# Kernel tuning notes

Hardware: AMD Instinct MI355X
Metric: run time of the kernel (lower is better)

The kernel has to match this reference:

```python
import jax, jax.numpy as jnp
import numpy as np

# FCHL19 hyperparameters (from init_kwargs defaults)
NSPEC = 4
RCUT = 6.0
NRS2 = 24
NRS3 = 20
ETA2 = 0.32
ETA3 = 2.7
TWO_BODY_DECAY = 1.8
THREE_BODY_WEIGHT = float(np.sqrt(2.7 / np.pi) * 13.4)  # sqrt(eta3/pi)*13.4, as in __init__
THREE_BODY_DECAY = 0.57
PI = float(np.pi)
NPAIRS = NSPEC * (NSPEC + 1) // 2  # 10 unordered element pairs
RS2 = jnp.linspace(0.0, RCUT, NRS2 + 1)[1:]
RS3 = jnp.linspace(0.0, RCUT, NRS3 + 1)[1:]


def setup_inputs() -> dict:
    key = jax.random.key(0)
    k1, k2, k3 = jax.random.split(key, 3)
    B, A = 64, 48
    X = jax.random.uniform(k1, (B, A, 3), jnp.float32, 0.0, 12.0)  # coords in 12 A box
    Z = jax.random.randint(k2, (B, A), 0, NSPEC, dtype=jnp.int32)  # species indices into [1,6,7,8]
    atom_counts = jax.random.randint(k3, (B,), 24, A + 1, dtype=jnp.int32)
    atomIDs = (jnp.arange(B * A, dtype=jnp.int32) % A)
    molIDs = (jnp.arange(B * A, dtype=jnp.int32) // A)
    return {"X": X, "Z": Z, "atomIDs": atomIDs, "molIDs": molIDs, "atom_counts": atom_counts}


def _fchl_rep(X, Z, atom_counts):
    B, A, _ = X.shape
    idx = jnp.arange(A)
    valid = idx[None, :] < atom_counts[:, None]                       # [B,A]
    diff = X[:, :, None, :] - X[:, None, :, :]                        # [B,A,A,3] (X_i - X_j)
    r2 = jnp.sum(diff * diff, axis=-1)
    eye = jnp.eye(A, dtype=bool)
    pmask = valid[:, :, None] & valid[:, None, :] & ~eye              # [B,A,A]
    r = jnp.sqrt(jnp.where(pmask, r2, 1.0))
    within = pmask & (r < RCUT)
    rs = jnp.where(within, r, 1.0)                                    # safe distances
    fc = jnp.where(within, 0.5 * (jnp.cos(PI * rs / RCUT) + 1.0), 0.0)

    # ---- two-body: log-normal radial basis with power-law scaling ----
    s2 = jnp.log1p(ETA2 / (rs * rs))                                  # sigma^2
    mu = jnp.log(rs) - 0.5 * s2
    pref = fc / (rs ** TWO_BODY_DECAY) / (jnp.sqrt(s2) * np.sqrt(2.0 * PI))
    radial2 = (pref[..., None] / RS2) * jnp.exp(
        -(jnp.log(RS2) - mu[..., None]) ** 2 / (2.0 * s2[..., None]))  # [B,A,A,nRs2]
    eoh = jax.nn.one_hot(Z, NSPEC, dtype=X.dtype) * valid[..., None]  # [B,A,S]
    rep2 = jnp.einsum('bijk,bjs->bisk', radial2, eoh).reshape(B, A, NSPEC * NRS2)

    # ---- three-body: ATM-weighted radial x (cos,sin) angular, pairs k>j ----
    rij = rs[:, :, :, None]   # [B,A(i),A(j),1]
    rik = rs[:, :, None, :]   # [B,A(i),1,A(k)]
    rjk = rs[:, None, :, :]   # [B,1,A(j),A(k)]
    cos_i = jnp.einsum('bijx,bikx->bijk', diff, diff) / (rij * rik)
    cos_i = jnp.clip(cos_i, -1.0, 1.0)
    cos_j = (rij * rij + rjk * rjk - rik * rik) / (2.0 * rij * rjk)
    cos_k = (rik * rik + rjk * rjk - rij * rij) / (2.0 * rik * rjk)
    mask3 = (within[:, :, :, None] & within[:, :, None, :]
             & (idx[None, :] > idx[:, None])[None, None, :, :])        # k > j
    ksi3 = THREE_BODY_WEIGHT * (1.0 + 3.0 * cos_i * cos_j * cos_k) \
        / (rij * rik * rjk) ** THREE_BODY_DECAY
    w = jnp.where(mask3, ksi3 * fc[:, :, :, None] * fc[:, :, None, :], 0.0)
    wc = w * cos_i
    ws = w * jnp.sqrt(jnp.clip(1.0 - cos_i * cos_i, 0.0, 1.0))
    d = 0.5 * (rij + rik)                                             # [B,A,A,A]

    # unordered element-pair bin for (Z_j, Z_k)
    ej = Z[:, :, None]
    ek = Z[:, None, :]
    pmin = jnp.minimum(ej, ek)
    pmax = jnp.maximum(ej, ek)
    pidx = pmin * (2 * NSPEC - pmin - 1) // 2 + pmax                  # [B,A,A]
    poh = jax.nn.one_hot(pidx, NPAIRS, dtype=X.dtype)                 # [B,A,A,P]

    def step(carry, Rl):
        rad = jnp.exp(-ETA3 * (d - Rl) ** 2)
        rc = jnp.einsum('bijk,bjkp->bip', wc * rad, poh)
        rsn = jnp.einsum('bijk,bjkp->bip', ws * rad, poh)
        return carry, jnp.stack([rc, rsn], axis=-1)                   # [B,A,P,2]

    _, rep3 = jax.lax.scan(step, 0, RS3)                              # [nRs3,B,A,P,2]
    rep3 = jnp.transpose(rep3, (1, 2, 3, 0, 4)).reshape(B, A, NPAIRS * NRS3 * 2)
    return jnp.concatenate([rep2, rep3], axis=-1)                     # [B,A,496]


def reference(X, Z, atomIDs, molIDs, atom_counts):
    # atomIDs/molIDs are CUDA work-distribution lists; math-irrelevant here.
    return _fchl_rep(X, Z, atom_counts)
```

## Files before the change

### kernel.cpp

```cpp
#include <hip/hip_runtime.h>
#include <math.h>

#define B_MOL 64
#define A_MAX 48
#define NSPEC 4
#define NRS2 24
#define NRS3 20
#define NPAIRS 10
#define REP2 (NSPEC * NRS2)
#define REP3 (NPAIRS * NRS3 * 2)
#define REPTOT (REP2 + REP3)
#define TRIP_CAP 1084

#define RCUT_F 6.0f
#define ETA2_F 0.32f
#define ETA3_F 2.7f
#define PI_F 3.14159265358979323846f
#define W3_F 12.4225780586f
#define SQRT_2PI_F 2.5066282746310002f

__device__ __forceinline__ void decode_tri(int t, int m, int& a_out, int& c_out) {
    const float fm = (float)(2 * m - 1);
    const float disc = fm * fm - 8.0f * (float)t;
    const float sq = __builtin_amdgcn_sqrtf(disc);
    int a = (int)((fm - sq) * 0.5f);
    if (a < 0) a = 0;
    while (a > 0 && (a * (2 * m - 1 - a)) / 2 > t) --a;
    while (((a + 1) * (2 * m - 1 - (a + 1))) / 2 <= t) ++a;
    a_out = a;
    c_out = t - (a * (2 * m - 1 - a)) / 2 + a + 1;
}

__global__ __launch_bounds__(256, 8) void fchl_kernel(
    const float* __restrict__ X, const int* __restrict__ Z,
    const int* __restrict__ atom_counts, float* __restrict__ out)
{
    const int bi = blockIdx.x;
    const int b = bi / A_MAX;
    const int i = bi % A_MAX;
    const int tid = threadIdx.x;

    __shared__ float nb_dx[A_MAX], nb_dy[A_MAX], nb_dz[A_MAX];
    __shared__ float nb_r[A_MAX], nb_r2[A_MAX], nb_rinv[A_MAX];
    __shared__ float nb_fc[A_MAX], nb_mu[A_MAX], nb_i2s2[A_MAX], nb_pref[A_MAX];
    __shared__ int   nb_z[A_MAX];
    __shared__ int   nb_m;
    __shared__ int   bcnt[NPAIRS], bstart[NPAIRS];
    __shared__ unsigned short pq[TRIP_CAP];
    __shared__ float trip_wc[TRIP_CAP], trip_ws[TRIP_CAP], trip_d[TRIP_CAP];

    const int cnt = atom_counts[b];
    float* orow = out + (size_t)bi * REPTOT;

    if (i >= cnt) {
        for (int t = tid; t < REPTOT; t += 256) orow[t] = 0.0f;
        return;
    }

    if (tid < NPAIRS) bcnt[tid] = 0;

    const float xi = X[(b * A_MAX + i) * 3 + 0];
    const float yi = X[(b * A_MAX + i) * 3 + 1];
    const float zi = X[(b * A_MAX + i) * 3 + 2];

    if (tid < 64) {
        const int j = tid;
        bool flag = false;
        float dx = 0.f, dy = 0.f, dz = 0.f, r = 1.f;
        int zj = 0;
        if (j < A_MAX && j < cnt) {
            dx = xi - X[(b * A_MAX + j) * 3 + 0];
            dy = yi - X[(b * A_MAX + j) * 3 + 1];
            dz = zi - X[(b * A_MAX + j) * 3 + 2];
            zj = Z[b * A_MAX + j];
            r = __builtin_amdgcn_sqrtf(dx * dx + dy * dy + dz * dz);
            flag = (j != i) && (r < RCUT_F);
        }
        const unsigned long long mask = __ballot(flag ? 1 : 0);
        if (flag) {
            const int pos = __popcll(mask & ((1ull << tid) - 1ull));
            nb_dx[pos] = dx; nb_dy[pos] = dy; nb_dz[pos] = dz;
            nb_r[pos]  = r;  nb_r2[pos] = r * r;
            nb_rinv[pos] = __builtin_amdgcn_rcpf(r);
            nb_z[pos]  = zj;
            const float fc = 0.5f * (__cosf(PI_F * r * (1.0f / RCUT_F)) + 1.0f);
            const float lr = __logf(r);
            const float s2 = log1pf(ETA2_F / (r * r));
            nb_fc[pos]   = fc;
            nb_mu[pos]   = lr - 0.5f * s2;
            nb_i2s2[pos] = 0.5f * __builtin_amdgcn_rcpf(s2);
            nb_pref[pos] = fc * __expf(-1.8f * lr) *
                           __builtin_amdgcn_rcpf(__builtin_amdgcn_sqrtf(s2) * SQRT_2PI_F);
        }
        if (tid == 0) nb_m = (int)__popcll(mask);
    }
    __syncthreads();
    const int m = nb_m;
    const int ntrip = m * (m - 1) / 2;

    for (int t = tid; t < ntrip; t += 256) {
        int a, c;
        decode_tri(t, m, a, c);
        const int zj = nb_z[a], zk = nb_z[c];
        const int pmn = min(zj, zk), pmx = max(zj, zk);
        const int p = (pmn * (2 * NSPEC - pmn - 1)) / 2 + pmx;
        const int q = atomicAdd(&bcnt[p], 1);
        pq[t] = (unsigned short)(p | (q << 4));
    }
    __syncthreads();
    if (tid < NPAIRS) {
        int s = 0;
        for (int p = 0; p < tid; ++p) s += bcnt[p];
        bstart[tid] = s;
    }
    __syncthreads();

    for (int t = tid; t < ntrip; t += 256) {
        int a, c;
        decode_tri(t, m, a, c);

        const float rij = nb_r[a], rik = nb_r[c];
        const float r2ij = nb_r2[a], r2ik = nb_r2[c];
        const float rinv_a = nb_rinv[a], rinv_c = nb_rinv[c];
        const float djx = nb_dx[a], djy = nb_dy[a], djz = nb_dz[a];
        const float dkx = nb_dx[c], dky = nb_dy[c], dkz = nb_dz[c];

        float cosi = (djx * dkx + djy * dky + djz * dkz) * rinv_a * rinv_c;
        cosi = fminf(1.0f, fmaxf(-1.0f, cosi));

        const float ex = dkx - djx, ey = dky - djy, ez = dkz - djz;
        const float rjk2 = ex * ex + ey * ey + ez * ez;
        const float rjk = __builtin_amdgcn_sqrtf(rjk2);
        const bool w_jk = (rjk < RCUT_F);
        const float rjke  = w_jk ? rjk : 1.0f;
        const float rjke2 = w_jk ? rjk2 : 1.0f;
        const float rinv_jk = w_jk ? __builtin_amdgcn_rcpf(rjk) : 1.0f;

        const float cosj = (r2ij + rjke2 - r2ik) * 0.5f * rinv_a * rinv_jk;
        const float cosk = (r2ik + rjke2 - r2ij) * 0.5f * rinv_c * rinv_jk;

        const float ksi = W3_F * (1.0f + 3.0f * cosi * cosj * cosk)
                        * __expf(-0.57f * __logf(rij * rik * rjke));
        const float w  = ksi * nb_fc[a] * nb_fc[c];
        const float wc = w * cosi;
        const float s1 = fmaxf(1.0f - cosi * cosi, 0.0f);
        const float ws = w * __builtin_amdgcn_sqrtf(s1);
        const float d  = 0.5f * (rij + rik);

        const unsigned short e = pq[t];
        const int slot = bstart[e & 15] + (int)(e >> 4);
        trip_wc[slot] = wc; trip_ws[slot] = ws; trip_d[slot] = d;
    }
    __syncthreads();

    if (tid < NPAIRS * NRS3) {
        const int p = tid / NRS3;
        const int l = tid % NRS3;
        const float Rl = 0.3f * (float)(l + 1);
        const int s0 = bstart[p];
        const int s1 = s0 + bcnt[p];
        float ac = 0.0f, as_ = 0.0f;
        if (s1 > s0) {
            float wcv = trip_wc[s0], wsv = trip_ws[s0], dv = trip_d[s0];
            for (int s = s0 + 1; s < s1; ++s) {
                const float wcn = trip_wc[s];
                const float wsn = trip_ws[s];
                const float dn  = trip_d[s];
                const float dd = dv - Rl;
                const float rad = __expf(-ETA3_F * dd * dd);
                ac  += wcv * rad;
                as_ += wsv * rad;
                wcv = wcn; wsv = wsn; dv = dn;
            }
            const float dd = dv - Rl;
            const float rad = __expf(-ETA3_F * dd * dd);
            ac  += wcv * rad;
            as_ += wsv * rad;
        }
        orow[REP2 + p * (NRS3 * 2) + l * 2 + 0] = ac;
        orow[REP2 + p * (NRS3 * 2) + l * 2 + 1] = as_;
    } else {
        for (int t2 = tid - 200; t2 < REP2; t2 += 56) {
            const int s = t2 / NRS2;
            const int n = t2 % NRS2;
            const float Rn = 0.25f * (float)(n + 1);
            const float logRn = __logf(Rn);
            float acc = 0.0f;
            for (int a = 0; a < m; ++a) {
                if (nb_z[a] == s) {
                    const float dmu = logRn - nb_mu[a];
                    acc += nb_pref[a] * __expf(-dmu * dmu * nb_i2s2[a]);
                }
            }
            orow[t2] = acc * __builtin_amdgcn_rcpf(Rn);
        }
    }
}

extern "C" void kernel_launch(void* const* d_in, const int* in_sizes, int n_in,
                              void* d_out, int out_size, void* d_ws, size_t ws_size,
                              hipStream_t stream) {
    const float* X           = (const float*)d_in[0];
    const int*   Z           = (const int*)d_in[1];
    const int*   atom_counts = (const int*)d_in[4];
    float* out = (float*)d_out;

    fchl_kernel<<<B_MOL * A_MAX, 256, 0, stream>>>(X, Z, atom_counts, out);
}
```

Measured before the change: 74.70 us.

## Map one wavefront per atom and accumulate three-body bins with LDS atomics

Restructures the kernel so each 64-lane wavefront handles one atom, with two atoms per block, replacing the 256-thread block per atom. The two-pass bucket sort of triplets by element pair (counting atomics, prefix sum, scatter) and the separate per-bin reduction are removed. Each lane instead computes a triplet and scatters its 20 radial contributions into a per-wave LDS accumulator with float atomics, starting at a lane-staggered offset to spread bank conflicts. This cuts block-wide barriers and idle threads, but adds many LDS atomic adds and puts all triplet work on 64 lanes per atom.

```diff
diff --git a/kernel.cpp b/kernel.cpp
--- a/kernel.cpp
+++ b/kernel.cpp
@@ -10,7 +10,6 @@
 #define REP2 (NSPEC * NRS2)
 #define REP3 (NPAIRS * NRS3 * 2)
 #define REPTOT (REP2 + REP3)
-#define TRIP_CAP 1084
 
 #define RCUT_F 6.0f
 #define ETA2_F 0.32f
@@ -18,6 +17,8 @@
 #define PI_F 3.14159265358979323846f
 #define W3_F 12.4225780586f
 #define SQRT_2PI_F 2.5066282746310002f
+
+#define WPB 2
 
 __device__ __forceinline__ void decode_tri(int t, int m, int& a_out, int& c_out) {
     const float fm = (float)(2 * m - 1);
@@ -31,169 +32,138 @@
     c_out = t - (a * (2 * m - 1 - a)) / 2 + a + 1;
 }
 
-__global__ __launch_bounds__(256, 8) void fchl_kernel(
+__global__ __launch_bounds__(64 * WPB, 6) void fchl_kernel(
     const float* __restrict__ X, const int* __restrict__ Z,
     const int* __restrict__ atom_counts, float* __restrict__ out)
 {
-    const int bi = blockIdx.x;
+    __shared__ float nb_dx[WPB][A_MAX], nb_dy[WPB][A_MAX], nb_dz[WPB][A_MAX];
+    __shared__ float nb_r[WPB][A_MAX], nb_r2[WPB][A_MAX], nb_rinv[WPB][A_MAX];
+    __shared__ float nb_fc[WPB][A_MAX], nb_mu[WPB][A_MAX];
+    __shared__ float nb_i2s2[WPB][A_MAX], nb_pref[WPB][A_MAX];
+    __shared__ int   nb_z[WPB][A_MAX];
+    __shared__ float acc3[WPB][REP3];
+
+    const int wv   = threadIdx.x >> 6;
+    const int lane = threadIdx.x & 63;
+    const int bi   = blockIdx.x * WPB + wv;
     const int b = bi / A_MAX;
     const int i = bi % A_MAX;
-    const int tid = threadIdx.x;
-
-    __shared__ float nb_dx[A_MAX], nb_dy[A_MAX], nb_dz[A_MAX];
-    __shared__ float nb_r[A_MAX], nb_r2[A_MAX], nb_rinv[A_MAX];
-    __shared__ float nb_fc[A_MAX], nb_mu[A_MAX], nb_i2s2[A_MAX], nb_pref[A_MAX];
-    __shared__ int   nb_z[A_MAX];
-    __shared__ int   nb_m;
-    __shared__ int   bcnt[NPAIRS], bstart[NPAIRS];
-    __shared__ unsigned short pq[TRIP_CAP];
-    __shared__ float trip_wc[TRIP_CAP], trip_ws[TRIP_CAP], trip_d[TRIP_CAP];
-
     const int cnt = atom_counts[b];
     float* orow = out + (size_t)bi * REPTOT;
+    const bool active = (i < cnt);
 
-    if (i >= cnt) {
-        for (int t = tid; t < REPTOT; t += 256) orow[t] = 0.0f;
-        return;
-    }
+    int m = 0;
 
-    if (tid < NPAIRS) bcnt[tid] = 0;
+    if (active) {
+        const float xi = X[(b * A_MAX + i) * 3 + 0];
+        const float yi = X[(b * A_MAX + i) * 3 + 1];
+        const float zi = X[(b * A_MAX + i) * 3 + 2];
 
-    const float xi = X[(b * A_MAX + i) * 3 + 0];
-    const float yi = X[(b * A_MAX + i) * 3 + 1];
-    const float zi = X[(b * A_MAX + i) * 3 + 2];
-
-    if (tid < 64) {
-        const int j = tid;
         bool flag = false;
         float dx = 0.f, dy = 0.f, dz = 0.f, r = 1.f;
         int zj = 0;
-        if (j < A_MAX && j < cnt) {
-            dx = xi - X[(b * A_MAX + j) * 3 + 0];
-            dy = yi - X[(b * A_MAX + j) * 3 + 1];
-            dz = zi - X[(b * A_MAX + j) * 3 + 2];
-            zj = Z[b * A_MAX + j];
+        if (lane < A_MAX && lane < cnt) {
+            dx = xi - X[(b * A_MAX + lane) * 3 + 0];
+            dy = yi - X[(b * A_MAX + lane) * 3 + 1];
+            dz = zi - X[(b * A_MAX + lane) * 3 + 2];
+            zj = Z[b * A_MAX + lane];
             r = __builtin_amdgcn_sqrtf(dx * dx + dy * dy + dz * dz);
-            flag = (j != i) && (r < RCUT_F);
+            flag = (lane != i) && (r < RCUT_F);
         }
         const unsigned long long mask = __ballot(flag ? 1 : 0);
         if (flag) {
-            const int pos = __popcll(mask & ((1ull << tid) - 1ull));
-            nb_dx[pos] = dx; nb_dy[pos] = dy; nb_dz[pos] = dz;
-            nb_r[pos]  = r;  nb_r2[pos] = r * r;
-            nb_rinv[pos] = __builtin_amdgcn_rcpf(r);
-            nb_z[pos]  = zj;
+            const int pos = __popcll(mask & ((1ull << lane) - 1ull));
+            nb_dx[wv][pos] = dx; nb_dy[wv][pos] = dy; nb_dz[wv][pos] = dz;
+            nb_r[wv][pos]  = r;  nb_r2[wv][pos] = r * r;
+            nb_rinv[wv][pos] = __builtin_amdgcn_rcpf(r);
+            nb_z[wv][pos]  = zj;
             const float fc = 0.5f * (__cosf(PI_F * r * (1.0f / RCUT_F)) + 1.0f);
             const float lr = __logf(r);
             const float s2 = log1pf(ETA2_F / (r * r));
-            nb_fc[pos]   = fc;
-            nb_mu[pos]   = lr - 0.5f * s2;
-            nb_i2s2[pos] = 0.5f * __builtin_amdgcn_rcpf(s2);
-            nb_pref[pos] = fc * __expf(-1.8f * lr) *
-                           __builtin_amdgcn_rcpf(__builtin_amdgcn_sqrtf(s2) * SQRT_2PI_F);
+            nb_fc[wv][pos]   = fc;
+            nb_mu[wv][pos]   = lr - 0.5f * s2;
+            nb_i2s2[wv][pos] = 0.5f * __builtin_amdgcn_rcpf(s2);
+            nb_pref[wv][pos] = fc * __expf(-1.8f * lr) *
+                               __builtin_amdgcn_rcpf(__builtin_amdgcn_sqrtf(s2) * SQRT_2PI_F);
         }
-        if (tid == 0) nb_m = (int)__popcll(mask);
-    }
-    __syncthreads();
-    const int m = nb_m;
-    const int ntrip = m * (m - 1) / 2;
-
-    for (int t = tid; t < ntrip; t += 256) {
-        int a, c;
-        decode_tri(t, m, a, c);
-        const int zj = nb_z[a], zk = nb_z[c];
-        const int pmn = min(zj, zk), pmx = max(zj, zk);
-        const int p = (pmn * (2 * NSPEC - pmn - 1)) / 2 + pmx;
-        const int q = atomicAdd(&bcnt[p], 1);
-        pq[t] = (unsigned short)(p | (q << 4));
-    }
-    __syncthreads();
-    if (tid < NPAIRS) {
-        int s = 0;
-        for (int p = 0; p < tid; ++p) s += bcnt[p];
-        bstart[tid] = s;
+        m = (int)__popcll(mask);
+        for (int k2 = lane; k2 < REP3; k2 += 64) acc3[wv][k2] = 0.0f;
     }
     __syncthreads();
 
-    for (int t = tid; t < ntrip; t += 256) {
-        int a, c;
-        decode_tri(t, m, a, c);
-
-        const float rij = nb_r[a], rik = nb_r[c];
-        const float r2ij = nb_r2[a], r2ik = nb_r2[c];
-        const float rinv_a = nb_rinv[a], rinv_c = nb_rinv[c];
-        const float djx = nb_dx[a], djy = nb_dy[a], djz = nb_dz[a];
-        const float dkx = nb_dx[c], dky = nb_dy[c], dkz = nb_dz[c];
-
-        float cosi = (djx * dkx + djy * dky + djz * dkz) * rinv_a * rinv_c;
-        cosi = fminf(1.0f, fmaxf(-1.0f, cosi));
-
-        const float ex = dkx - djx, ey = dky - djy, ez = dkz - djz;
-        const float rjk2 = ex * ex + ey * ey + ez * ez;
-        const float rjk = __builtin_amdgcn_sqrtf(rjk2);
-        const bool w_jk = (rjk < RCUT_F);
-        const float rjke  = w_jk ? rjk : 1.0f;
-        const float rjke2 = w_jk ? rjk2 : 1.0f;
-        const float rinv_jk = w_jk ? __builtin_amdgcn_rcpf(rjk) : 1.0f;
-
-        const float cosj = (r2ij + rjke2 - r2ik) * 0.5f * rinv_a * rinv_jk;
-        const float cosk = (r2ik + rjke2 - r2ij) * 0.5f * rinv_c * rinv_jk;
-
-        const float ksi = W3_F * (1.0f + 3.0f * cosi * cosj * cosk)
-                        * __expf(-0.57f * __logf(rij * rik * rjke));
-        const float w  = ksi * nb_fc[a] * nb_fc[c];
-        const float wc = w * cosi;
-        const float s1 = fmaxf(1.0f - cosi * cosi, 0.0f);
-        const float ws = w * __builtin_amdgcn_sqrtf(s1);
-        const float d  = 0.5f * (rij + rik);
-
-        const unsigned short e = pq[t];
-        const int slot = bstart[e & 15] + (int)(e >> 4);
-        trip_wc[slot] = wc; trip_ws[slot] = ws; trip_d[slot] = d;
-    }
-    __syncthreads();
-
-    if (tid < NPAIRS * NRS3) {
-        const int p = tid / NRS3;
-        const int l = tid % NRS3;
-        const float Rl = 0.3f * (float)(l + 1);
-        const int s0 = bstart[p];
-        const int s1 = s0 + bcnt[p];
-        float ac = 0.0f, as_ = 0.0f;
-        if (s1 > s0) {
-            float wcv = trip_wc[s0], wsv = trip_ws[s0], dv = trip_d[s0];
-            for (int s = s0 + 1; s < s1; ++s) {
-                const float wcn = trip_wc[s];
-                const float wsn = trip_ws[s];
-                const float dn  = trip_d[s];
-                const float dd = dv - Rl;
-                const float rad = __expf(-ETA3_F * dd * dd);
-                ac  += wcv * rad;
-                as_ += wsv * rad;
-                wcv = wcn; wsv = wsn; dv = dn;
-            }
-            const float dd = dv - Rl;
-            const float rad = __expf(-ETA3_F * dd * dd);
-            ac  += wcv * rad;
-            as_ += wsv * rad;
-        }
-        orow[REP2 + p * (NRS3 * 2) + l * 2 + 0] = ac;
-        orow[REP2 + p * (NRS3 * 2) + l * 2 + 1] = as_;
-    } else {
-        for (int t2 = tid - 200; t2 < REP2; t2 += 56) {
+    if (active) {
+        for (int t2 = lane; t2 < REP2; t2 += 64) {
             const int s = t2 / NRS2;
             const int n = t2 % NRS2;
             const float Rn = 0.25f * (float)(n + 1);
             const float logRn = __logf(Rn);
             float acc = 0.0f;
             for (int a = 0; a < m; ++a) {
-                if (nb_z[a] == s) {
-                    const float dmu = logRn - nb_mu[a];
-                    acc += nb_pref[a] * __expf(-dmu * dmu * nb_i2s2[a]);
+                if (nb_z[wv][a] == s) {
+                    const float dmu = logRn - nb_mu[wv][a];
+                    acc += nb_pref[wv][a] * __expf(-dmu * dmu * nb_i2s2[wv][a]);
                 }
             }
             orow[t2] = acc * __builtin_amdgcn_rcpf(Rn);
         }
+
+        const int ntrip = m * (m - 1) / 2;
+        const int l0 = lane % NRS3;
+        for (int t = lane; t < ntrip; t += 64) {
+            int a, c;
+            decode_tri(t, m, a, c);
+
+            const float rij = nb_r[wv][a], rik = nb_r[wv][c];
+            const float r2ij = nb_r2[wv][a], r2ik = nb_r2[wv][c];
+            const float rinv_a = nb_rinv[wv][a], rinv_c = nb_rinv[wv][c];
+            const float djx = nb_dx[wv][a], djy = nb_dy[wv][a], djz = nb_dz[wv][a];
+            const float dkx = nb_dx[wv][c], dky = nb_dy[wv][c], dkz = nb_dz[wv][c];
+
+            float cosi = (djx * dkx + djy * dky + djz * dkz) * rinv_a * rinv_c;
+            cosi = fminf(1.0f, fmaxf(-1.0f, cosi));
+
+            const float ex = dkx - djx, ey = dky - djy, ez = dkz - djz;
+            const float rjk2 = ex * ex + ey * ey + ez * ez;
+            const float rjk = __builtin_amdgcn_sqrtf(rjk2);
+            const bool w_jk = (rjk < RCUT_F);
+            const float rjke  = w_jk ? rjk : 1.0f;
+            const float rjke2 = w_jk ? rjk2 : 1.0f;
+            const float rinv_jk = w_jk ? __builtin_amdgcn_rcpf(rjk) : 1.0f;
+
+            const float cosj = (r2ij + rjke2 - r2ik) * 0.5f * rinv_a * rinv_jk;
+            const float cosk = (r2ik + rjke2 - r2ij) * 0.5f * rinv_c * rinv_jk;
+
+            const float ksi = W3_F * (1.0f + 3.0f * cosi * cosj * cosk)
+                            * __expf(-0.57f * __logf(rij * rik * rjke));
+            const float w  = ksi * nb_fc[wv][a] * nb_fc[wv][c];
+            const float wc = w * cosi;
+            const float s1 = fmaxf(1.0f - cosi * cosi, 0.0f);
+            const float ws = w * __builtin_amdgcn_sqrtf(s1);
+            const float d  = 0.5f * (rij + rik);
+
+            const int zj = nb_z[wv][a], zk = nb_z[wv][c];
+            const int pmn = min(zj, zk), pmx = max(zj, zk);
+            const int p = (pmn * (2 * NSPEC - pmn - 1)) / 2 + pmx;
+            float* accp = &acc3[wv][p * (NRS3 * 2)];
+
+            int l = l0;
+            for (int it = 0; it < NRS3; ++it) {
+                const float Rl = 0.3f * (float)(l + 1);
+                const float dd = d - Rl;
+                const float rad = __expf(-ETA3_F * dd * dd);
+                atomicAdd(&accp[2 * l + 0], wc * rad);
+                atomicAdd(&accp[2 * l + 1], ws * rad);
+                l = (l + 1 == NRS3) ? 0 : l + 1;
+            }
+        }
+    } else {
+        for (int k2 = lane; k2 < REPTOT; k2 += 64) orow[k2] = 0.0f;
+    }
+    __syncthreads();
+
+    if (active) {
+        for (int k2 = lane; k2 < REP3; k2 += 64)
+            orow[REP2 + k2] = acc3[wv][k2];
     }
 }
 
@@ -205,5 +175,5 @@
     const int*   atom_counts = (const int*)d_in[4];
     float* out = (float*)d_out;
 
-    fchl_kernel<<<B_MOL * A_MAX, 256, 0, stream>>>(X, Z, atom_counts, out);
+    fchl_kernel<<<(B_MOL * A_MAX) / WPB, 64 * WPB, 0, stream>>>(X, Z, atom_counts, out);
 }
```

Result: slower. 121.7 us (+62.9%).

## Use single-wavefront blocks and bin triplets via an index list in one pass

Applied to the files above, without the earlier changes.

Shrinks each block from 256 threads to a single 64-lane wavefront, so the neighbour count comes straight from a ballot and no shared broadcast is needed. The triplet loop now computes weights, stores them in natural order and does the pair-bin atomic in the same pass, which removes the second decode pass. A separate scatter then builds a sorted index array that the three-body accumulation reads indirectly. Each block now has a quarter of the threads for the same work, which trades parallelism within a block for fewer redundant decodes. The accumulation loop also pays an extra indirect LDS load for every triplet.

```diff
diff --git a/kernel.cpp b/kernel.cpp
--- a/kernel.cpp
+++ b/kernel.cpp
@@ -31,54 +31,52 @@
     c_out = t - (a * (2 * m - 1 - a)) / 2 + a + 1;
 }
 
-__global__ __launch_bounds__(256, 8) void fchl_kernel(
+__global__ __launch_bounds__(64, 4) void fchl_kernel(
     const float* __restrict__ X, const int* __restrict__ Z,
     const int* __restrict__ atom_counts, float* __restrict__ out)
 {
-    const int bi = blockIdx.x;
-    const int b = bi / A_MAX;
-    const int i = bi % A_MAX;
-    const int tid = threadIdx.x;
-
     __shared__ float nb_dx[A_MAX], nb_dy[A_MAX], nb_dz[A_MAX];
     __shared__ float nb_r[A_MAX], nb_r2[A_MAX], nb_rinv[A_MAX];
     __shared__ float nb_fc[A_MAX], nb_mu[A_MAX], nb_i2s2[A_MAX], nb_pref[A_MAX];
     __shared__ int   nb_z[A_MAX];
-    __shared__ int   nb_m;
-    __shared__ int   bcnt[NPAIRS], bstart[NPAIRS];
+    __shared__ float trip_wc[TRIP_CAP], trip_ws[TRIP_CAP], trip_d[TRIP_CAP];
     __shared__ unsigned short pq[TRIP_CAP];
-    __shared__ float trip_wc[TRIP_CAP], trip_ws[TRIP_CAP], trip_d[TRIP_CAP];
-
+    __shared__ unsigned short sidx[TRIP_CAP];
+    __shared__ int bcnt[NPAIRS], bstart[NPAIRS];
+
+    const int bi = blockIdx.x;
+    const int b = bi / A_MAX;
+    const int i = bi % A_MAX;
+    const int lane = threadIdx.x;
     const int cnt = atom_counts[b];
     float* orow = out + (size_t)bi * REPTOT;
 
     if (i >= cnt) {
-        for (int t = tid; t < REPTOT; t += 256) orow[t] = 0.0f;
+        for (int t = lane; t < REPTOT; t += 64) orow[t] = 0.0f;
         return;
     }
 
-    if (tid < NPAIRS) bcnt[tid] = 0;
+    if (lane < NPAIRS) bcnt[lane] = 0;
 
     const float xi = X[(b * A_MAX + i) * 3 + 0];
     const float yi = X[(b * A_MAX + i) * 3 + 1];
     const float zi = X[(b * A_MAX + i) * 3 + 2];
 
-    if (tid < 64) {
-        const int j = tid;
-        bool flag = false;
+    bool flag = false;
+    {
         float dx = 0.f, dy = 0.f, dz = 0.f, r = 1.f;
         int zj = 0;
-        if (j < A_MAX && j < cnt) {
-            dx = xi - X[(b * A_MAX + j) * 3 + 0];
-            dy = yi - X[(b * A_MAX + j) * 3 + 1];
-            dz = zi - X[(b * A_MAX + j) * 3 + 2];
-            zj = Z[b * A_MAX + j];
+        if (lane < A_MAX && lane < cnt) {
+            dx = xi - X[(b * A_MAX + lane) * 3 + 0];
+            dy = yi - X[(b * A_MAX + lane) * 3 + 1];
+            dz = zi - X[(b * A_MAX + lane) * 3 + 2];
+            zj = Z[b * A_MAX + lane];
             r = __builtin_amdgcn_sqrtf(dx * dx + dy * dy + dz * dz);
-            flag = (j != i) && (r < RCUT_F);
+            flag = (lane != i) && (r < RCUT_F);
         }
         const unsigned long long mask = __ballot(flag ? 1 : 0);
         if (flag) {
-            const int pos = __popcll(mask & ((1ull << tid) - 1ull));
+            const int pos = __popcll(mask & ((1ull << lane) - 1ull));
             nb_dx[pos] = dx; nb_dy[pos] = dy; nb_dz[pos] = dz;
             nb_r[pos]  = r;  nb_r2[pos] = r * r;
             nb_rinv[pos] = __builtin_amdgcn_rcpf(r);
@@ -92,30 +90,27 @@
             nb_pref[pos] = fc * __expf(-1.8f * lr) *
                            __builtin_amdgcn_rcpf(__builtin_amdgcn_sqrtf(s2) * SQRT_2PI_F);
         }
-        if (tid == 0) nb_m = (int)__popcll(mask);
-    }
-    __syncthreads();
-    const int m = nb_m;
+    }
+    const int m = (int)__popcll(__ballot(flag ? 1 : 0));
+    __syncthreads();
+
+    for (int t2 = lane; t2 < REP2; t2 += 64) {
+        const int s = t2 / NRS2;
+        const int n = t2 % NRS2;
+        const float Rn = 0.25f * (float)(n + 1);
+        const float logRn = __logf(Rn);
+        float acc = 0.0f;
+        for (int a = 0; a < m; ++a) {
+            if (nb_z[a] == s) {
+                const float dmu = logRn - nb_mu[a];
+                acc += nb_pref[a] * __expf(-dmu * dmu * nb_i2s2[a]);
+            }
+        }
+        orow[t2] = acc * __builtin_amdgcn_rcpf(Rn);
+    }
+
     const int ntrip = m * (m - 1) / 2;
-
-    for (int t = tid; t < ntrip; t += 256) {
-        int a, c;
-        decode_tri(t, m, a, c);
-        const int zj = nb_z[a], zk = nb_z[c];
-        const int pmn = min(zj, zk), pmx = max(zj, zk);
-        const int p = (pmn * (2 * NSPEC - pmn - 1)) / 2 + pmx;
-        const int q = atomicAdd(&bcnt[p], 1);
-        pq[t] = (unsigned short)(p | (q << 4));
-    }
-    __syncthreads();
-    if (tid < NPAIRS) {
-        int s = 0;
-        for (int p = 0; p < tid; ++p) s += bcnt[p];
-        bstart[tid] = s;
-    }
-    __syncthreads();
-
-    for (int t = tid; t < ntrip; t += 256) {
+    for (int t = lane; t < ntrip; t += 64) {
         int a, c;
         decode_tri(t, m, a, c);
 
@@ -142,58 +137,58 @@
         const float ksi = W3_F * (1.0f + 3.0f * cosi * cosj * cosk)
                         * __expf(-0.57f * __logf(rij * rik * rjke));
         const float w  = ksi * nb_fc[a] * nb_fc[c];
-        const float wc = w * cosi;
         const float s1 = fmaxf(1.0f - cosi * cosi, 0.0f);
-        const float ws = w * __builtin_amdgcn_sqrtf(s1);
-        const float d  = 0.5f * (rij + rik);
-
+
+        trip_wc[t] = w * cosi;
+        trip_ws[t] = w * __builtin_amdgcn_sqrtf(s1);
+        trip_d[t]  = 0.5f * (rij + rik);
+
+        const int zj = nb_z[a], zk = nb_z[c];
+        const int pmn = min(zj, zk), pmx = max(zj, zk);
+        const int p = (pmn * (2 * NSPEC - pmn - 1)) / 2 + pmx;
+        const int q = atomicAdd(&bcnt[p], 1);
+        pq[t] = (unsigned short)(p | (q << 4));
+    }
+    __syncthreads();
+    if (lane < NPAIRS) {
+        int s = 0;
+        for (int p = 0; p < lane; ++p) s += bcnt[p];
+        bstart[lane] = s;
+    }
+    __syncthreads();
+
+    for (int t = lane; t < ntrip; t += 64) {
         const unsigned short e = pq[t];
-        const int slot = bstart[e & 15] + (int)(e >> 4);
-        trip_wc[slot] = wc; trip_ws[slot] = ws; trip_d[slot] = d;
-    }
-    __syncthreads();
-
-    if (tid < NPAIRS * NRS3) {
-        const int p = tid / NRS3;
-        const int l = tid % NRS3;
+        sidx[bstart[e & 15] + (int)(e >> 4)] = (unsigned short)t;
+    }
+    __syncthreads();
+
+    for (int e = lane; e < NPAIRS * NRS3; e += 64) {
+        const int p = e / NRS3;
+        const int l = e % NRS3;
         const float Rl = 0.3f * (float)(l + 1);
         const int s0 = bstart[p];
         const int s1 = s0 + bcnt[p];
         float ac = 0.0f, as_ = 0.0f;
         if (s1 > s0) {
-            float wcv = trip_wc[s0], wsv = trip_ws[s0], dv = trip_d[s0];
+            int idx = sidx[s0];
             for (int s = s0 + 1; s < s1; ++s) {
-                const float wcn = trip_wc[s];
-                const float wsn = trip_ws[s];
-                const float dn  = trip_d[s];
+                const int idxn = sidx[s];
+                const float dv = trip_d[idx];
                 const float dd = dv - Rl;
                 const float rad = __expf(-ETA3_F * dd * dd);
-                ac  += wcv * rad;
-                as_ += wsv * rad;
-                wcv = wcn; wsv = wsn; dv = dn;
+                ac  += trip_wc[idx] * rad;
+                as_ += trip_ws[idx] * rad;
+                idx = idxn;
             }
+            const float dv = trip_d[idx];
             const float dd = dv - Rl;
             const float rad = __expf(-ETA3_F * dd * dd);
-            ac  += wcv * rad;
-            as_ += wsv * rad;
+            ac  += trip_wc[idx] * rad;
+            as_ += trip_ws[idx] * rad;
         }
         orow[REP2 + p * (NRS3 * 2) + l * 2 + 0] = ac;
         orow[REP2 + p * (NRS3 * 2) + l * 2 + 1] = as_;
-    } else {
-        for (int t2 = tid - 200; t2 < REP2; t2 += 56) {
-            const int s = t2 / NRS2;
-            const int n = t2 % NRS2;
-            const float Rn = 0.25f * (float)(n + 1);
-            const float logRn = __logf(Rn);
-            float acc = 0.0f;
-            for (int a = 0; a < m; ++a) {
-                if (nb_z[a] == s) {
-                    const float dmu = logRn - nb_mu[a];
-                    acc += nb_pref[a] * __expf(-dmu * dmu * nb_i2s2[a]);
-                }
-            }
-            orow[t2] = acc * __builtin_amdgcn_rcpf(Rn);
-        }
     }
 }
 
@@ -205,5 +200,5 @@
     const int*   atom_counts = (const int*)d_in[4];
     float* out = (float*)d_out;
 
-    fchl_kernel<<<B_MOL * A_MAX, 256, 0, stream>>>(X, Z, atom_counts, out);
+    fchl_kernel<<<B_MOL * A_MAX, 64, 0, stream>>>(X, Z, atom_counts, out);
 }
```

New measurement: 85.00 us. +13.8%, slower.

## Compute triplet bin slots analytically from per-species ballots, dropping atomic binning pass

Applied to the files above, without the earlier changes.

Replaces the atomic-counting pass that bucketed triplets by element pair with closed-form slot indices. Per-species ballots give each neighbour its rank within its species and the count of each species, so slot offsets and ranks come from arithmetic. This removes one triplet loop, the shared atomics and two block barriers. The radial accumulation loop is also unrolled by two with split accumulators to raise instruction-level parallelism. The bin order inside each pair is now deterministic, which changes the float summation order.

```diff
diff --git a/kernel.cpp b/kernel.cpp
--- a/kernel.cpp
+++ b/kernel.cpp
@@ -35,20 +35,18 @@
     const float* __restrict__ X, const int* __restrict__ Z,
     const int* __restrict__ atom_counts, float* __restrict__ out)
 {
+    __shared__ float nb_dx[A_MAX], nb_dy[A_MAX], nb_dz[A_MAX];
+    __shared__ float nb_r[A_MAX], nb_r2[A_MAX], nb_rinv[A_MAX];
+    __shared__ float nb_fc[A_MAX], nb_mu[A_MAX], nb_i2s2[A_MAX], nb_pref[A_MAX];
+    __shared__ int   nb_z[A_MAX], nb_si[A_MAX];
+    __shared__ float trip_wc[TRIP_CAP], trip_ws[TRIP_CAP], trip_d[TRIP_CAP];
+    __shared__ int   cnt_s[NSPEC];
+    __shared__ int   nb_m;
+
     const int bi = blockIdx.x;
     const int b = bi / A_MAX;
     const int i = bi % A_MAX;
     const int tid = threadIdx.x;
-
-    __shared__ float nb_dx[A_MAX], nb_dy[A_MAX], nb_dz[A_MAX];
-    __shared__ float nb_r[A_MAX], nb_r2[A_MAX], nb_rinv[A_MAX];
-    __shared__ float nb_fc[A_MAX], nb_mu[A_MAX], nb_i2s2[A_MAX], nb_pref[A_MAX];
-    __shared__ int   nb_z[A_MAX];
-    __shared__ int   nb_m;
-    __shared__ int   bcnt[NPAIRS], bstart[NPAIRS];
-    __shared__ unsigned short pq[TRIP_CAP];
-    __shared__ float trip_wc[TRIP_CAP], trip_ws[TRIP_CAP], trip_d[TRIP_CAP];
-
     const int cnt = atom_counts[b];
     float* orow = out + (size_t)bi * REPTOT;
 
@@ -57,32 +55,37 @@
         return;
     }
 
-    if (tid < NPAIRS) bcnt[tid] = 0;
-
-    const float xi = X[(b * A_MAX + i) * 3 + 0];
-    const float yi = X[(b * A_MAX + i) * 3 + 1];
-    const float zi = X[(b * A_MAX + i) * 3 + 2];
-
     if (tid < 64) {
-        const int j = tid;
+        const float xi = X[(b * A_MAX + i) * 3 + 0];
+        const float yi = X[(b * A_MAX + i) * 3 + 1];
+        const float zi = X[(b * A_MAX + i) * 3 + 2];
+
         bool flag = false;
         float dx = 0.f, dy = 0.f, dz = 0.f, r = 1.f;
         int zj = 0;
-        if (j < A_MAX && j < cnt) {
-            dx = xi - X[(b * A_MAX + j) * 3 + 0];
-            dy = yi - X[(b * A_MAX + j) * 3 + 1];
-            dz = zi - X[(b * A_MAX + j) * 3 + 2];
-            zj = Z[b * A_MAX + j];
+        if (tid < A_MAX && tid < cnt) {
+            dx = xi - X[(b * A_MAX + tid) * 3 + 0];
+            dy = yi - X[(b * A_MAX + tid) * 3 + 1];
+            dz = zi - X[(b * A_MAX + tid) * 3 + 2];
+            zj = Z[b * A_MAX + tid];
             r = __builtin_amdgcn_sqrtf(dx * dx + dy * dy + dz * dz);
-            flag = (j != i) && (r < RCUT_F);
-        }
-        const unsigned long long mask = __ballot(flag ? 1 : 0);
+            flag = (tid != i) && (r < RCUT_F);
+        }
+        const unsigned long long ms0 = __ballot(flag && zj == 0);
+        const unsigned long long ms1 = __ballot(flag && zj == 1);
+        const unsigned long long ms2 = __ballot(flag && zj == 2);
+        const unsigned long long ms3 = __ballot(flag && zj == 3);
+        const unsigned long long mask = ms0 | ms1 | ms2 | ms3;
         if (flag) {
-            const int pos = __popcll(mask & ((1ull << tid) - 1ull));
+            const unsigned long long below = (1ull << tid) - 1ull;
+            const int pos = __popcll(mask & below);
             nb_dx[pos] = dx; nb_dy[pos] = dy; nb_dz[pos] = dz;
             nb_r[pos]  = r;  nb_r2[pos] = r * r;
             nb_rinv[pos] = __builtin_amdgcn_rcpf(r);
             nb_z[pos]  = zj;
+            const unsigned long long msp = (zj == 0) ? ms0 : (zj == 1) ? ms1
+                                         : (zj == 2) ? ms2 : ms3;
+            nb_si[pos] = __popcll(msp & below);
             const float fc = 0.5f * (__cosf(PI_F * r * (1.0f / RCUT_F)) + 1.0f);
             const float lr = __logf(r);
             const float s2 = log1pf(ETA2_F / (r * r));
@@ -92,28 +95,25 @@
             nb_pref[pos] = fc * __expf(-1.8f * lr) *
                            __builtin_amdgcn_rcpf(__builtin_amdgcn_sqrtf(s2) * SQRT_2PI_F);
         }
-        if (tid == 0) nb_m = (int)__popcll(mask);
+        if (tid == 0) {
+            cnt_s[0] = (int)__popcll(ms0);
+            cnt_s[1] = (int)__popcll(ms1);
+            cnt_s[2] = (int)__popcll(ms2);
+            cnt_s[3] = (int)__popcll(ms3);
+            nb_m = (int)__popcll(mask);
+        }
     }
     __syncthreads();
-    const int m = nb_m;
+
+    const int m  = nb_m;
+    const int c0 = cnt_s[0], c1 = cnt_s[1], c2 = cnt_s[2], c3 = cnt_s[3];
+    const int S0 = (c0 * (c0 - 1)) >> 1;
+    const int S1 = c0 * c1, S2 = c0 * c2, S3 = c0 * c3;
+    const int S4 = (c1 * (c1 - 1)) >> 1;
+    const int S5 = c1 * c2, S6 = c1 * c3;
+    const int S7 = (c2 * (c2 - 1)) >> 1;
+    const int S8 = c2 * c3;
     const int ntrip = m * (m - 1) / 2;
-
-    for (int t = tid; t < ntrip; t += 256) {
-        int a, c;
-        decode_tri(t, m, a, c);
-        const int zj = nb_z[a], zk = nb_z[c];
-        const int pmn = min(zj, zk), pmx = max(zj, zk);
-        const int p = (pmn * (2 * NSPEC - pmn - 1)) / 2 + pmx;
-        const int q = atomicAdd(&bcnt[p], 1);
-        pq[t] = (unsigned short)(p | (q << 4));
-    }
-    __syncthreads();
-    if (tid < NPAIRS) {
-        int s = 0;
-        for (int p = 0; p < tid; ++p) s += bcnt[p];
-        bstart[tid] = s;
-    }
-    __syncthreads();
 
     for (int t = tid; t < ntrip; t += 256) {
         int a, c;
@@ -142,14 +142,32 @@
         const float ksi = W3_F * (1.0f + 3.0f * cosi * cosj * cosk)
                         * __expf(-0.57f * __logf(rij * rik * rjke));
         const float w  = ksi * nb_fc[a] * nb_fc[c];
-        const float wc = w * cosi;
-        const float s1 = fmaxf(1.0f - cosi * cosi, 0.0f);
-        const float ws = w * __builtin_amdgcn_sqrtf(s1);
-        const float d  = 0.5f * (rij + rik);
-
-        const unsigned short e = pq[t];
-        const int slot = bstart[e & 15] + (int)(e >> 4);
-        trip_wc[slot] = wc; trip_ws[slot] = ws; trip_d[slot] = d;
+        const float s1v = fmaxf(1.0f - cosi * cosi, 0.0f);
+
+        const int za = nb_z[a], zc = nb_z[c];
+        const int ia = nb_si[a], ic = nb_si[c];
+        const int pmn = min(za, zc), pmx = max(za, zc);
+        const int p = (pmn * (2 * NSPEC - pmn - 1)) / 2 + pmx;
+        int rank;
+        if (za == zc) {
+            const int cs = (za == 0) ? c0 : (za == 1) ? c1 : (za == 2) ? c2 : c3;
+            rank = ia * cs - ((ia * (ia + 1)) >> 1) + (ic - ia - 1);
+        } else {
+            const int cmx = (pmx == 0) ? c0 : (pmx == 1) ? c1 : (pmx == 2) ? c2 : c3;
+            const int iu = (za < zc) ? ia : ic;
+            const int iv = (za < zc) ? ic : ia;
+            rank = iu * cmx + iv;
+        }
+        int slot = rank;
+        slot += (p > 0) ? S0 : 0;  slot += (p > 1) ? S1 : 0;
+        slot += (p > 2) ? S2 : 0;  slot += (p > 3) ? S3 : 0;
+        slot += (p > 4) ? S4 : 0;  slot += (p > 5) ? S5 : 0;
+        slot += (p > 6) ? S6 : 0;  slot += (p > 7) ? S7 : 0;
+        slot += (p > 8) ? S8 : 0;
+
+        trip_wc[slot] = w * cosi;
+        trip_ws[slot] = w * __builtin_amdgcn_sqrtf(s1v);
+        trip_d[slot]  = 0.5f * (rij + rik);
     }
     __syncthreads();
 
@@ -157,37 +175,44 @@
         const int p = tid / NRS3;
         const int l = tid % NRS3;
         const float Rl = 0.3f * (float)(l + 1);
-        const int s0 = bstart[p];
-        const int s1 = s0 + bcnt[p];
-        float ac = 0.0f, as_ = 0.0f;
-        if (s1 > s0) {
-            float wcv = trip_wc[s0], wsv = trip_ws[s0], dv = trip_d[s0];
-            for (int s = s0 + 1; s < s1; ++s) {
-                const float wcn = trip_wc[s];
-                const float wsn = trip_ws[s];
-                const float dn  = trip_d[s];
-                const float dd = dv - Rl;
-                const float rad = __expf(-ETA3_F * dd * dd);
-                ac  += wcv * rad;
-                as_ += wsv * rad;
-                wcv = wcn; wsv = wsn; dv = dn;
-            }
-            const float dd = dv - Rl;
-            const float rad = __expf(-ETA3_F * dd * dd);
-            ac  += wcv * rad;
-            as_ += wsv * rad;
-        }
-        orow[REP2 + p * (NRS3 * 2) + l * 2 + 0] = ac;
-        orow[REP2 + p * (NRS3 * 2) + l * 2 + 1] = as_;
+        int s0 = 0;
+        s0 += (p > 0) ? S0 : 0;  s0 += (p > 1) ? S1 : 0;
+        s0 += (p > 2) ? S2 : 0;  s0 += (p > 3) ? S3 : 0;
+        s0 += (p > 4) ? S4 : 0;  s0 += (p > 5) ? S5 : 0;
+        s0 += (p > 6) ? S6 : 0;  s0 += (p > 7) ? S7 : 0;
+        s0 += (p > 8) ? S8 : 0;
+        const int sz = (p == 0) ? S0 : (p == 1) ? S1 : (p == 2) ? S2
+                     : (p == 3) ? S3 : (p == 4) ? S4 : (p == 5) ? S5
+                     : (p == 6) ? S6 : (p == 7) ? S7 : (p == 8) ? S8
+                     : (ntrip - s0);
+        const int s1 = s0 + sz;
+
+        float ac0 = 0.0f, as0 = 0.0f, ac1 = 0.0f, as1 = 0.0f;
+        int s = s0;
+        for (; s + 1 < s1; s += 2) {
+            const float d0 = trip_d[s],     d1 = trip_d[s + 1];
+            const float dd0 = d0 - Rl,      dd1 = d1 - Rl;
+            const float e0 = __expf(-ETA3_F * dd0 * dd0);
+            const float e1 = __expf(-ETA3_F * dd1 * dd1);
+            ac0 += trip_wc[s] * e0;     as0 += trip_ws[s] * e0;
+            ac1 += trip_wc[s + 1] * e1; as1 += trip_ws[s + 1] * e1;
+        }
+        if (s < s1) {
+            const float dd = trip_d[s] - Rl;
+            const float e = __expf(-ETA3_F * dd * dd);
+            ac0 += trip_wc[s] * e;  as0 += trip_ws[s] * e;
+        }
+        orow[REP2 + p * (NRS3 * 2) + l * 2 + 0] = ac0 + ac1;
+        orow[REP2 + p * (NRS3 * 2) + l * 2 + 1] = as0 + as1;
     } else {
         for (int t2 = tid - 200; t2 < REP2; t2 += 56) {
-            const int s = t2 / NRS2;
+            const int sp = t2 / NRS2;
             const int n = t2 % NRS2;
             const float Rn = 0.25f * (float)(n + 1);
             const float logRn = __logf(Rn);
             float acc = 0.0f;
             for (int a = 0; a < m; ++a) {
-                if (nb_z[a] == s) {
+                if (nb_z[a] == sp) {
                     const float dmu = logRn - nb_mu[a];
                     acc += nb_pref[a] * __expf(-dmu * dmu * nb_i2s2[a]);
                 }
```

After: 73.57 us. No clear change (-1.5%).
